# Optimization experiments

Hardware: AMD Instinct MI355X
Metric: run time of the kernel (lower is better)

Reference implementation:

```python
import jax, jax.numpy as jnp
import numpy as np

T, B_SZ = 1024, 1024
NX, NU, ND, NM, NDT, NH = 128, 64, 32, 32, 32, 128


def setup_inputs() -> dict:
    key = jax.random.key(0)
    ks = jax.random.split(key, 10)
    return {
        "x": jax.random.normal(ks[0], (B_SZ, NX), jnp.float32),
        "M_flow": jax.random.normal(ks[1], (T, B_SZ, NM), jnp.float32),
        "DT": jax.random.normal(ks[2], (T, B_SZ, NDT), jnp.float32),
        "D": jax.random.normal(ks[3], (T, B_SZ, ND), jnp.float32),
        # ConstrainedLinear(nx, nx): weight and scalar init with torch.rand -> uniform[0,1)
        "A_weight": jax.random.uniform(ks[4], (NX, NX), jnp.float32),
        "A_scalar": jax.random.uniform(ks[5], (NX, NX), jnp.float32),
        # nn.Linear(in, out, bias=False) weights are [out, in]
        "B_w": jax.random.normal(ks[6], (NX, NU), jnp.float32) * (1.0 / np.sqrt(NU)),
        "E_w": jax.random.normal(ks[7], (NX, ND), jnp.float32) * (1.0 / np.sqrt(ND)),
        "hf1_w": jax.random.normal(ks[8], (NH, NM + NDT), jnp.float32) * (1.0 / np.sqrt(NM + NDT)),
        "hf2_w": jax.random.normal(ks[9], (NU, NH), jnp.float32) * (1.0 / np.sqrt(NH)),
    }


def reference(x, M_flow, DT, D, A_weight, A_scalar, B_w, E_w, hf1_w, hf2_w):
    # Constrained weight: ((1 - 0.1*sigmoid(scalar)) * softmax(weight, dim=1)).T
    # It is constant across time, so compute once (torch redundantly recomputes it per step).
    s_clamped = 1.0 - 0.1 * jax.nn.sigmoid(A_scalar)
    W_eff = (s_clamped * jax.nn.softmax(A_weight, axis=1)).T  # [nx, nx]

    # Per-step control input u_t depends only on exogenous M_flow/DT -> vectorize over time.
    md = jnp.concatenate([M_flow, DT], axis=2)                # [T, B, n_m+n_dT]
    h = jax.nn.relu(jnp.einsum('tbi,hi->tbh', md, hf1_w))     # [T, B, n_hidden]
    u = jax.nn.relu(jnp.einsum('tbh,uh->tbu', h, hf2_w))      # [T, B, nu]

    # Precompute additive drive B(u_t) + E(d_t); only x@W_eff is sequential.
    drive = jnp.einsum('tbu,xu->tbx', u, B_w) + jnp.einsum('tbd,xd->tbx', D, E_w)

    def step(x_prev, drive_t):
        x_new = x_prev @ W_eff + drive_t
        return x_new, x_new

    _, X = jax.lax.scan(step, x, drive)  # X: [T, B, nx]
    Y = X[:, :, -1]                      # [T, B]
    return X, Y
```

## Files before the change

### kernel.cpp

```cpp
#include <hip/hip_runtime.h>

typedef _Float16 h4 __attribute__((ext_vector_type(4)));
typedef _Float16 h8 __attribute__((ext_vector_type(8)));
typedef float f4 __attribute__((ext_vector_type(4)));

#define MFMA16(a, b, c) __builtin_amdgcn_mfma_f32_16x16x32_f16((a), (b), (c), 0, 0, 0)

static constexpr int TT  = 1024;
static constexpr int BS  = 1024;
static constexpr int LCH = 32;
static constexpr int NCH = 32;
static constexpr size_t XTOT = (size_t)TT * BS * 128;

static constexpr size_t WS_WT16 = 0;
static constexpr size_t WS_HF1  = 32768;
static constexpr size_t WS_HF2  = 49152;
static constexpr size_t WS_BW   = 65536;
static constexpr size_t WS_EW   = 81920;
static constexpr size_t WS_W32  = 90112;
static constexpr size_t WS_F    = 131072;
static constexpr size_t WS_INIT = WS_F + (size_t)NCH * BS * 128 * 4;
static constexpr size_t WS_DRV  = WS_INIT + (size_t)NCH * BS * 128 * 4;

template <typename T>
__device__ inline T ntload(const T* p) { return __builtin_nontemporal_load(p); }

__global__ void prep_kernel(const float* __restrict__ Aw, const float* __restrict__ As,
                            const float* __restrict__ hf1, const float* __restrict__ hf2,
                            const float* __restrict__ Bw, const float* __restrict__ Ew,
                            char* __restrict__ ws)
{
    const int tid = threadIdx.x;
    const int bid = blockIdx.x;
    if (bid < 128) {
        __shared__ float red[128];
        const int n = bid;
        const float a = Aw[n * 128 + tid];
        red[tid] = a;
        __syncthreads();
        for (int s = 64; s > 0; s >>= 1) {
            if (tid < s) red[tid] = fmaxf(red[tid], red[tid + s]);
            __syncthreads();
        }
        const float mx = red[0];
        __syncthreads();
        const float e = expf(a - mx);
        red[tid] = e;
        __syncthreads();
        for (int s = 64; s > 0; s >>= 1) {
            if (tid < s) red[tid] += red[tid + s];
            __syncthreads();
        }
        const float sm  = e / red[0];
        const float asv = As[n * 128 + tid];
        const float sc  = 1.0f - 0.1f * (1.0f / (1.0f + expf(-asv)));
        ((_Float16*)(ws + WS_WT16))[n * 128 + tid] = (_Float16)(sc * sm);
    } else {
        const int b2 = bid - 128;
        for (int i = b2 * 128 + tid; i < 8192; i += 32 * 128) {
            ((_Float16*)(ws + WS_HF1))[i] = (_Float16)hf1[i];
            ((_Float16*)(ws + WS_HF2))[i] = (_Float16)hf2[i];
            ((_Float16*)(ws + WS_BW))[i]  = (_Float16)Bw[i];
            if (i < 4096) ((_Float16*)(ws + WS_EW))[i] = (_Float16)Ew[i];
        }
    }
}

__global__ void w32_kernel(char* __restrict__ ws)
{
    const int tid  = threadIdx.x;
    const int lane = tid & 63;
    const int w    = tid >> 6;
    const int cl   = lane & 15;
    const int gq   = lane >> 4;

    __shared__ __align__(16) _Float16 Ta[128 * 128];
    __shared__ __align__(16) _Float16 Tb[128 * 128];

    const _Float16* Wt16 = (const _Float16*)(ws + WS_WT16);
    for (int i = tid; i < 2048; i += 256)
        *(h8*)&Ta[i * 8] = *(const h8*)&Wt16[i * 8];
    __syncthreads();

    for (int s = 0; s < 5; ++s) {
        const _Float16* src = (s & 1) ? Tb : Ta;
        _Float16* dst       = (s & 1) ? Ta : Tb;
        f4 acc[8][2];
#pragma unroll
        for (int mt = 0; mt < 8; ++mt)
#pragma unroll
            for (int nt = 0; nt < 2; ++nt) acc[mt][nt] = f4{};
#pragma unroll
        for (int kk = 0; kk < 4; ++kk) {
            h8 b0, b1;
#pragma unroll
            for (int j = 0; j < 8; ++j) {
                const int kr = kk * 32 + gq * 8 + j;
                b0[j] = src[kr * 128 + w * 32 + cl];
                b1[j] = src[kr * 128 + w * 32 + 16 + cl];
            }
#pragma unroll
            for (int mt = 0; mt < 8; ++mt) {
                h8 a = *(const h8*)&src[(mt * 16 + cl) * 128 + kk * 32 + gq * 8];
                acc[mt][0] = MFMA16(a, b0, acc[mt][0]);
                acc[mt][1] = MFMA16(a, b1, acc[mt][1]);
            }
        }
        __syncthreads();
#pragma unroll
        for (int mt = 0; mt < 8; ++mt)
#pragma unroll
            for (int nt = 0; nt < 2; ++nt)
#pragma unroll
                for (int r = 0; r < 4; ++r)
                    dst[(mt * 16 + gq * 4 + r) * 128 + w * 32 + nt * 16 + cl] =
                        (_Float16)acc[mt][nt][r];
        __syncthreads();
    }
    _Float16* W32 = (_Float16*)(ws + WS_W32);
    for (int i = tid; i < 2048; i += 256)
        *(h8*)&W32[i * 8] = *(const h8*)&Tb[i * 8];
}

__global__ __launch_bounds__(256, 4)
void drive_kernel(const float* __restrict__ Mfl, const float* __restrict__ DTi,
                  const float* __restrict__ Din, char* __restrict__ ws)
{
    const int tid  = threadIdx.x;
    const int lane = tid & 63;
    const int w    = tid >> 6;
    const int cl   = lane & 15;
    const int gq   = lane >> 4;
    const int bt   = blockIdx.x & 63;
    const int tq   = blockIdx.x >> 6;
    const int b0   = bt * 16;

    const _Float16* Hf1  = (const _Float16*)(ws + WS_HF1);
    const _Float16* Hf2  = (const _Float16*)(ws + WS_HF2);
    const _Float16* Bw16 = (const _Float16*)(ws + WS_BW);
    const _Float16* Ew16 = (const _Float16*)(ws + WS_EW);
    _Float16* Drv        = (_Float16*)(ws + WS_DRV);

    __shared__ __align__(16) _Float16 mds[4][16 * 64];
    __shared__ __align__(16) _Float16 dts[4][16 * 32];
    __shared__ __align__(16) _Float16 hs[4][16 * 128];
    __shared__ __align__(16) _Float16 us[4][16 * 64];

    const int qrow = (tid & 127) >> 3;
    const int qc4  = (tid & 7) * 4;
    f4 pm[4], pd[4];
#pragma unroll
    for (int s = 0; s < 4; ++s) {
        const size_t t  = (size_t)tq * 4 + s;
        const size_t rb = (t * BS + b0 + qrow) * 32 + qc4;
        pm[s] = (tid < 128) ? ntload((const f4*)&Mfl[rb]) : ntload((const f4*)&DTi[rb]);
        if (tid < 128) pd[s] = ntload((const f4*)&Din[rb]);
    }
#pragma unroll
    for (int s = 0; s < 4; ++s) {
        const int col = (tid < 128) ? qc4 : (32 + qc4);
        h4 hv;
#pragma unroll
        for (int j = 0; j < 4; ++j) hv[j] = (_Float16)pm[s][j];
        *(h4*)&mds[s][qrow * 64 + (((col >> 3) ^ (qrow & 7)) * 8) + (col & 7)] = hv;
        if (tid < 128) {
            h4 h2;
#pragma unroll
            for (int j = 0; j < 4; ++j) h2[j] = (_Float16)pd[s][j];
            *(h4*)&dts[s][qrow * 32 + (((qc4 >> 3) ^ (qrow & 3)) * 8) + (qc4 & 7)] = h2;
        }
    }

    h8 hf1f[2][2], bwf[2][2], ewf[2], hf2f[4];
#pragma unroll
    for (int nt = 0; nt < 2; ++nt) {
        const int ng = w * 32 + nt * 16 + cl;
#pragma unroll
        for (int kk = 0; kk < 2; ++kk) {
            hf1f[nt][kk] = *(const h8*)&Hf1[ng * 64 + kk * 32 + gq * 8];
            bwf[nt][kk]  = *(const h8*)&Bw16[ng * 64 + kk * 32 + gq * 8];
        }
        ewf[nt] = *(const h8*)&Ew16[ng * 32 + gq * 8];
    }
    {
        const int ng = w * 16 + cl;
#pragma unroll
        for (int kk = 0; kk < 4; ++kk)
            hf2f[kk] = *(const h8*)&Hf2[ng * 128 + kk * 32 + gq * 8];
    }
    __syncthreads();

#pragma unroll
    for (int s = 0; s < 4; ++s) {
        f4 ha[2] = {};
#pragma unroll
        for (int kk = 0; kk < 2; ++kk) {
            h8 a = *(const h8*)&mds[s][cl * 64 + (((kk * 4 + gq) ^ (cl & 7)) * 8)];
            ha[0] = MFMA16(hf1f[0][kk], a, ha[0]);
            ha[1] = MFMA16(hf1f[1][kk], a, ha[1]);
        }
#pragma unroll
        for (int nt = 0; nt < 2; ++nt) {
            const int nb8 = w * 4 + nt * 2 + (gq >> 1);
            h4 hv;
#pragma unroll
            for (int r = 0; r < 4; ++r) hv[r] = (_Float16)fmaxf(ha[nt][r], 0.f);
            *(h4*)&hs[s][cl * 128 + ((nb8 ^ cl) & 15) * 8 + (gq & 1) * 4] = hv;
        }
    }
    __syncthreads();

#pragma unroll
    for (int s = 0; s < 4; ++s) {
        f4 ua = {};
#pragma unroll
        for (int kt = 0; kt < 4; ++kt) {
            h8 a = *(const h8*)&hs[s][cl * 128 + (((kt * 4 + gq) ^ cl) & 15) * 8];
            ua = MFMA16(hf2f[kt], a, ua);
        }
        const int nb8 = w * 2 + (gq >> 1);
        h4 hv;
#pragma unroll
        for (int r = 0; r < 4; ++r) hv[r] = (_Float16)fmaxf(ua[r], 0.f);
        *(h4*)&us[s][cl * 64 + ((nb8 ^ (cl & 7)) & 7) * 8 + (gq & 1) * 4] = hv;
    }
    __syncthreads();

#pragma unroll
    for (int s = 0; s < 4; ++s) {
        f4 acc[2] = {};
#pragma unroll
        for (int kk = 0; kk < 2; ++kk) {
            h8 a = *(const h8*)&us[s][cl * 64 + (((kk * 4 + gq) ^ (cl & 7)) & 7) * 8];
            acc[0] = MFMA16(bwf[0][kk], a, acc[0]);
            acc[1] = MFMA16(bwf[1][kk], a, acc[1]);
        }
        {
            h8 a = *(const h8*)&dts[s][cl * 32 + ((gq ^ (cl & 3)) * 8)];
            acc[0] = MFMA16(ewf[0], a, acc[0]);
            acc[1] = MFMA16(ewf[1], a, acc[1]);
        }
        h8 o;
#pragma unroll
        for (int r = 0; r < 4; ++r) { o[r] = (_Float16)acc[0][r]; o[4 + r] = (_Float16)acc[1][r]; }
        const size_t t = (size_t)tq * 4 + s;
        *(h8*)&Drv[((t * 64 + bt) * 256 + tid) * 8] = o;
    }
}

template <bool FINAL>
__global__ __launch_bounds__(256, 2)
void scan_kernel(char* __restrict__ ws,
                 float* __restrict__ Xout, float* __restrict__ Yout)
{
    const int wslot = threadIdx.x >> 6;
    const int wid   = blockIdx.x * 4 + wslot;
    const int lane  = threadIdx.x & 63;
    const int cl = lane & 15, gq = lane >> 4;
    const int c  = wid >> 6;
    const int bt = wid & 63;
    const int b0 = bt * 16;

    const _Float16* Wt16 = (const _Float16*)(ws + WS_WT16);
    const _Float16* Drv  = (const _Float16*)(ws + WS_DRV);
    float* Fbuf       = (float*)(ws + WS_F);
    const float* Init = (const float*)(ws + WS_INIT);

    __shared__ __align__(16) _Float16 tb[4][16 * 128];
    _Float16* tbuf = tb[wslot];

    h8 wf[8][4];
#pragma unroll
    for (int nt = 0; nt < 8; ++nt)
#pragma unroll
        for (int kt = 0; kt < 4; ++kt)
            wf[nt][kt] = *(const h8*)&Wt16[(nt * 16 + cl) * 128 + kt * 32 + gq * 8];

    h8 xf[4];
    if constexpr (FINAL) {
        f4 iv[8];
#pragma unroll
        for (int nt = 0; nt < 8; ++nt)
            iv[nt] = *(const f4*)&Init[((size_t)c * BS + b0 + cl) * 128 + nt * 16 + gq * 4];
#pragma unroll
        for (int nt = 0; nt < 8; ++nt) {
            h4 hv;
#pragma unroll
            for (int r = 0; r < 4; ++r) hv[r] = (_Float16)iv[nt][r];
            *(h4*)&tbuf[cl * 128 + (((nt * 2 + (gq >> 1)) ^ cl) & 15) * 8 + (gq & 1) * 4] = hv;
        }
#pragma unroll
        for (int kt = 0; kt < 4; ++kt)
            xf[kt] = *(const h8*)&tbuf[cl * 128 + (((kt * 4 + gq) ^ cl) & 15) * 8];
    } else {
#pragma unroll
        for (int kt = 0; kt < 4; ++kt) xf[kt] = h8{};
    }

    constexpr size_t STEP = 16384;
    const h8* dp = (const h8*)Drv + (((size_t)(c * LCH) * 64 + bt) * 4) * 64 + lane;
    h8 dra0, dra1, dra2, dra3, drb0, drb1, drb2, drb3;
    dra0 = dp[0];          dra1 = dp[64];          dra2 = dp[128];          dra3 = dp[192];
    drb0 = dp[STEP];       drb1 = dp[STEP + 64];   drb2 = dp[STEP + 128];   drb3 = dp[STEP + 192];

#define SCAN_STEP(K, D0, D1, D2, D3)                                                     \
    {                                                                                    \
        f4 acc[8];                                                                       \
        _Pragma("unroll") for (int r = 0; r < 4; ++r) {                                  \
            acc[0][r] = (float)D0[r]; acc[1][r] = (float)D0[4 + r];                      \
            acc[2][r] = (float)D1[r]; acc[3][r] = (float)D1[4 + r];                      \
            acc[4][r] = (float)D2[r]; acc[5][r] = (float)D2[4 + r];                      \
            acc[6][r] = (float)D3[r]; acc[7][r] = (float)D3[4 + r];                      \
        }                                                                                \
        if ((K) + 2 < LCH) {                                                             \
            D0 = dp[(size_t)((K) + 2) * STEP + 0];                                       \
            D1 = dp[(size_t)((K) + 2) * STEP + 64];                                      \
            D2 = dp[(size_t)((K) + 2) * STEP + 128];                                     \
            D3 = dp[(size_t)((K) + 2) * STEP + 192];                                     \
        }                                                                                \
        _Pragma("unroll") for (int kt = 0; kt < 4; ++kt)                                 \
            _Pragma("unroll") for (int nt = 0; nt < 8; ++nt)                             \
                acc[nt] = MFMA16(wf[nt][kt], xf[kt], acc[nt]);                           \
        if constexpr (FINAL) {                                                           \
            const size_t t = (size_t)c * LCH + (K);                                      \
            float* xp = &Xout[(t * BS + b0 + cl) * 128 + gq * 4];                        \
            _Pragma("unroll") for (int nt = 0; nt < 8; ++nt)                             \
                __builtin_nontemporal_store(acc[nt], (f4*)&xp[nt * 16]);                 \
            if (gq == 3)                                                                 \
                __builtin_nontemporal_store(acc[7][3], &Yout[t * BS + b0 + cl]);         \
        } else if ((K) == LCH - 1) {                                                     \
            _Pragma("unroll") for (int nt = 0; nt < 8; ++nt)                             \
                *(f4*)&Fbuf[((size_t)c * BS + b0 + cl) * 128 + nt * 16 + gq * 4] =       \
                    acc[nt];                                                             \
        }                                                                                \
        if ((K) < LCH - 1) {                                                             \
            _Pragma("unroll") for (int nt = 0; nt < 8; ++nt) {                           \
                h4 hv;                                                                   \
                _Pragma("unroll") for (int r = 0; r < 4; ++r)                            \
                    hv[r] = (_Float16)acc[nt][r];                                        \
                *(h4*)&tbuf[cl * 128 + (((nt * 2 + (gq >> 1)) ^ cl) & 15) * 8 +          \
                            (gq & 1) * 4] = hv;                                          \
            }                                                                            \
            _Pragma("unroll") for (int kt = 0; kt < 4; ++kt)                             \
                xf[kt] = *(const h8*)&tbuf[cl * 128 + (((kt * 4 + gq) ^ cl) & 15) * 8];  \
        }                                                                                \
    }

    for (int k = 0; k < LCH; k += 2) {
        SCAN_STEP(k, dra0, dra1, dra2, dra3);
        SCAN_STEP(k + 1, drb0, drb1, drb2, drb3);
    }
#undef SCAN_STEP
}

__global__ __launch_bounds__(64, 1)
void carry_kernel(const float* __restrict__ x0, char* __restrict__ ws, int n_steps)
{
    const int lane = threadIdx.x;
    const int cl = lane & 15, gq = lane >> 4;
    const int b0 = blockIdx.x * 16;

    const _Float16* W32 = (const _Float16*)(ws + WS_W32);
    const float* Fbuf   = (const float*)(ws + WS_F);
    float* Init         = (float*)(ws + WS_INIT);

    __shared__ __align__(16) _Float16 tbuf[16 * 128];

    h8 wf[8][4];
#pragma unroll
    for (int nt = 0; nt < 8; ++nt)
#pragma unroll
        for (int kt = 0; kt < 4; ++kt)
            wf[nt][kt] = *(const h8*)&W32[(nt * 16 + cl) * 128 + kt * 32 + gq * 8];

    h8 xf[4];
    {
        f4 iv[8];
#pragma unroll
        for (int nt = 0; nt < 8; ++nt)
            iv[nt] = *(const f4*)&x0[(size_t)(b0 + cl) * 128 + nt * 16 + gq * 4];
#pragma unroll
        for (int nt = 0; nt < 8; ++nt)
            *(f4*)&Init[(size_t)(b0 + cl) * 128 + nt * 16 + gq * 4] = iv[nt];
#pragma unroll
        for (int nt = 0; nt < 8; ++nt) {
            h4 hv;
#pragma unroll
            for (int r = 0; r < 4; ++r) hv[r] = (_Float16)iv[nt][r];
            *(h4*)&tbuf[cl * 128 + (((nt * 2 + (gq >> 1)) ^ cl) & 15) * 8 + (gq & 1) * 4] = hv;
        }
#pragma unroll
        for (int kt = 0; kt < 4; ++kt)
            xf[kt] = *(const h8*)&tbuf[cl * 128 + (((kt * 4 + gq) ^ cl) & 15) * 8];
    }

    for (int cc = 1; cc <= n_steps; ++cc) {
        f4 acc[8];
#pragma unroll
        for (int nt = 0; nt < 8; ++nt)
            acc[nt] = *(const f4*)&Fbuf[((size_t)(cc - 1) * BS + b0 + cl) * 128 + nt * 16 + gq * 4];
#pragma unroll
        for (int kt = 0; kt < 4; ++kt)
#pragma unroll
            for (int nt = 0; nt < 8; ++nt)
                acc[nt] = MFMA16(wf[nt][kt], xf[kt], acc[nt]);
#pragma unroll
        for (int nt = 0; nt < 8; ++nt)
            *(f4*)&Init[((size_t)cc * BS + b0 + cl) * 128 + nt * 16 + gq * 4] = acc[nt];
        if (cc < n_steps) {
#pragma unroll
            for (int nt = 0; nt < 8; ++nt) {
                h4 hv;
#pragma unroll
                for (int r = 0; r < 4; ++r) hv[r] = (_Float16)acc[nt][r];
                *(h4*)&tbuf[cl * 128 + (((nt * 2 + (gq >> 1)) ^ cl) & 15) * 8 + (gq & 1) * 4] = hv;
            }
#pragma unroll
            for (int kt = 0; kt < 4; ++kt)
                xf[kt] = *(const h8*)&tbuf[cl * 128 + (((kt * 4 + gq) ^ cl) & 15) * 8];
        }
    }
}

extern "C" void kernel_launch(void* const* d_in, const int* in_sizes, int n_in,
                              void* d_out, int out_size, void* d_ws, size_t ws_size,
                              hipStream_t stream)
{
    const float* x_in = (const float*)d_in[0];
    const float* Mfl  = (const float*)d_in[1];
    const float* DTi  = (const float*)d_in[2];
    const float* Din  = (const float*)d_in[3];
    const float* Aw   = (const float*)d_in[4];
    const float* As   = (const float*)d_in[5];
    const float* Bw   = (const float*)d_in[6];
    const float* Ew   = (const float*)d_in[7];
    const float* hf1  = (const float*)d_in[8];
    const float* hf2  = (const float*)d_in[9];
    char* ws    = (char*)d_ws;
    float* Xout = (float*)d_out;
    float* Yout = Xout + XTOT;

    prep_kernel<<<dim3(160), dim3(128), 0, stream>>>(Aw, As, hf1, hf2, Bw, Ew, ws);
    w32_kernel<<<dim3(1), dim3(256), 0, stream>>>(ws);

    drive_kernel<<<dim3(256 * 64), dim3(256), 0, stream>>>(Mfl, DTi, Din, ws);
    scan_kernel<false><<<dim3(496), dim3(256), 0, stream>>>(ws, nullptr, nullptr);
    carry_kernel<<<dim3(64), dim3(64), 0, stream>>>(x_in, ws, 31);
    scan_kernel<true><<<dim3(512), dim3(256), 0, stream>>>(ws, Xout, Yout);
}
```

Baseline: 456.0 us.

## Fuse drive computation into chunked scan kernels and drop drive buffer

Removes the separate drive kernel and its fp16 drive buffer in workspace. Each scan block now recomputes the MLP drive for its chunk on the fly, with its 4 waves splitting the output columns and syncing through shared memory each step. The chunk scan runs twice (partial and final), so the drive MLP is computed twice and the per-step block barrier adds latency. In exchange, a large global write and read of drive data is avoided. The W^32 power kernel is also reworked to keep both transposed copies in padded shared memory so B-operand loads vectorize.

```diff
diff --git a/kernel.cpp b/kernel.cpp
--- a/kernel.cpp
+++ b/kernel.cpp
@@ -20,7 +20,6 @@
 static constexpr size_t WS_W32  = 90112;
 static constexpr size_t WS_F    = 131072;
 static constexpr size_t WS_INIT = WS_F + (size_t)NCH * BS * 128 * 4;
-static constexpr size_t WS_DRV  = WS_INIT + (size_t)NCH * BS * 128 * 4;
 
 template <typename T>
 __device__ inline T ntload(const T* p) { return __builtin_nontemporal_load(p); }
@@ -73,58 +72,76 @@
     const int w    = tid >> 6;
     const int cl   = lane & 15;
     const int gq   = lane >> 4;
-
-    __shared__ __align__(16) _Float16 Ta[128 * 128];
-    __shared__ __align__(16) _Float16 Tb[128 * 128];
+    constexpr int LDP = 136;
+
+    __shared__ __align__(16) _Float16 G[2][128 * LDP];
+    __shared__ __align__(16) _Float16 H[2][128 * LDP];
 
     const _Float16* Wt16 = (const _Float16*)(ws + WS_WT16);
     for (int i = tid; i < 2048; i += 256)
-        *(h8*)&Ta[i * 8] = *(const h8*)&Wt16[i * 8];
+        *(h8*)&G[0][(i >> 4) * LDP + (i & 15) * 8] = *(const h8*)&Wt16[i * 8];
     __syncthreads();
-
+    for (int i = tid; i < 16384; i += 256) {
+        const int r = i >> 7, cc = i & 127;
+        H[0][cc * LDP + r] = G[0][r * LDP + cc];
+    }
+    __syncthreads();
+
+    int cur = 0;
     for (int s = 0; s < 5; ++s) {
-        const _Float16* src = (s & 1) ? Tb : Ta;
-        _Float16* dst       = (s & 1) ? Ta : Tb;
-        f4 acc[8][2];
+        const _Float16* Gs = G[cur];
+        const _Float16* Hs = H[cur];
+        _Float16* Gd = G[cur ^ 1];
+        _Float16* Hd = H[cur ^ 1];
+        f4 aG[8][2], aH[8][2];
 #pragma unroll
         for (int mt = 0; mt < 8; ++mt)
 #pragma unroll
-            for (int nt = 0; nt < 2; ++nt) acc[mt][nt] = f4{};
+            for (int nt = 0; nt < 2; ++nt) { aG[mt][nt] = f4{}; aH[mt][nt] = f4{}; }
 #pragma unroll
         for (int kk = 0; kk < 4; ++kk) {
-            h8 b0, b1;
-#pragma unroll
-            for (int j = 0; j < 8; ++j) {
-                const int kr = kk * 32 + gq * 8 + j;
-                b0[j] = src[kr * 128 + w * 32 + cl];
-                b1[j] = src[kr * 128 + w * 32 + 16 + cl];
-            }
+            h8 bG0 = *(const h8*)&Hs[((w * 2 + 0) * 16 + cl) * LDP + kk * 32 + gq * 8];
+            h8 bG1 = *(const h8*)&Hs[((w * 2 + 1) * 16 + cl) * LDP + kk * 32 + gq * 8];
+            h8 bH0 = *(const h8*)&Gs[((w * 2 + 0) * 16 + cl) * LDP + kk * 32 + gq * 8];
+            h8 bH1 = *(const h8*)&Gs[((w * 2 + 1) * 16 + cl) * LDP + kk * 32 + gq * 8];
 #pragma unroll
             for (int mt = 0; mt < 8; ++mt) {
-                h8 a = *(const h8*)&src[(mt * 16 + cl) * 128 + kk * 32 + gq * 8];
-                acc[mt][0] = MFMA16(a, b0, acc[mt][0]);
-                acc[mt][1] = MFMA16(a, b1, acc[mt][1]);
-            }
-        }
-        __syncthreads();
+                h8 ag = *(const h8*)&Gs[(mt * 16 + cl) * LDP + kk * 32 + gq * 8];
+                h8 ah = *(const h8*)&Hs[(mt * 16 + cl) * LDP + kk * 32 + gq * 8];
+                aG[mt][0] = MFMA16(ag, bG0, aG[mt][0]);
+                aG[mt][1] = MFMA16(ag, bG1, aG[mt][1]);
+                aH[mt][0] = MFMA16(ah, bH0, aH[mt][0]);
+                aH[mt][1] = MFMA16(ah, bH1, aH[mt][1]);
+            }
+        }
 #pragma unroll
         for (int mt = 0; mt < 8; ++mt)
 #pragma unroll
-            for (int nt = 0; nt < 2; ++nt)
-#pragma unroll
-                for (int r = 0; r < 4; ++r)
-                    dst[(mt * 16 + gq * 4 + r) * 128 + w * 32 + nt * 16 + cl] =
-                        (_Float16)acc[mt][nt][r];
-        __syncthreads();
+            for (int nt = 0; nt < 2; ++nt) {
+                h4 hg, hh;
+#pragma unroll
+                for (int r = 0; r < 4; ++r) {
+                    hg[r] = (_Float16)aG[mt][nt][r];
+                    hh[r] = (_Float16)aH[mt][nt][r];
+                }
+                const int col  = (w * 2 + nt) * 16 + cl;
+                const int rowb = mt * 16 + gq * 4;
+                *(h4*)&Hd[col * LDP + rowb] = hg;
+                *(h4*)&Gd[col * LDP + rowb] = hh;
+            }
+        __syncthreads();
+        cur ^= 1;
     }
     _Float16* W32 = (_Float16*)(ws + WS_W32);
     for (int i = tid; i < 2048; i += 256)
-        *(h8*)&W32[i * 8] = *(const h8*)&Tb[i * 8];
+        *(h8*)&W32[i * 8] = *(const h8*)&G[cur][(i >> 4) * LDP + (i & 15) * 8];
 }
 
-__global__ __launch_bounds__(256, 4)
-void drive_kernel(const float* __restrict__ Mfl, const float* __restrict__ DTi,
-                  const float* __restrict__ Din, char* __restrict__ ws)
+template <bool FINAL>
+__global__ __launch_bounds__(256, 2)
+void fused_scan(const float* __restrict__ Mfl, const float* __restrict__ DTi,
+                const float* __restrict__ Din, char* __restrict__ ws,
+                float* __restrict__ Xout, float* __restrict__ Yout)
 {
     const int tid  = threadIdx.x;
     const int lane = tid & 63;
@@ -132,229 +149,206 @@
     const int cl   = lane & 15;
     const int gq   = lane >> 4;
     const int bt   = blockIdx.x & 63;
-    const int tq   = blockIdx.x >> 6;
+    const int c    = blockIdx.x >> 6;
     const int b0   = bt * 16;
 
     const _Float16* Hf1  = (const _Float16*)(ws + WS_HF1);
     const _Float16* Hf2  = (const _Float16*)(ws + WS_HF2);
     const _Float16* Bw16 = (const _Float16*)(ws + WS_BW);
     const _Float16* Ew16 = (const _Float16*)(ws + WS_EW);
-    _Float16* Drv        = (_Float16*)(ws + WS_DRV);
+    const _Float16* Wt16 = (const _Float16*)(ws + WS_WT16);
+    float* Fbuf          = (float*)(ws + WS_F);
+    const float* Init    = (const float*)(ws + WS_INIT);
 
     __shared__ __align__(16) _Float16 mds[4][16 * 64];
     __shared__ __align__(16) _Float16 dts[4][16 * 32];
     __shared__ __align__(16) _Float16 hs[4][16 * 128];
     __shared__ __align__(16) _Float16 us[4][16 * 64];
+    __shared__ __align__(16) _Float16 xsh[2][16 * 128];
+
+    h8 hf1f[2][2], bwf[2][2], ewf[2], hf2f[4];
+#pragma unroll
+    for (int nt = 0; nt < 2; ++nt) {
+        const int ng = w * 32 + nt * 16 + cl;
+#pragma unroll
+        for (int kk = 0; kk < 2; ++kk) {
+            hf1f[nt][kk] = *(const h8*)&Hf1[ng * 64 + kk * 32 + gq * 8];
+            bwf[nt][kk]  = *(const h8*)&Bw16[ng * 64 + kk * 32 + gq * 8];
+        }
+        ewf[nt] = *(const h8*)&Ew16[ng * 32 + gq * 8];
+    }
+    {
+        const int ng = w * 16 + cl;
+#pragma unroll
+        for (int kk = 0; kk < 4; ++kk)
+            hf2f[kk] = *(const h8*)&Hf2[ng * 128 + kk * 32 + gq * 8];
+    }
+    h8 wfp[2][4];
+#pragma unroll
+    for (int nt = 0; nt < 2; ++nt)
+#pragma unroll
+        for (int kt = 0; kt < 4; ++kt)
+            wfp[nt][kt] =
+                *(const h8*)&Wt16[(w * 32 + nt * 16 + cl) * 128 + kt * 32 + gq * 8];
+
+    if constexpr (FINAL) {
+        const int row = tid >> 4, c8 = tid & 15;
+        const float* src = &Init[((size_t)c * BS + b0 + row) * 128 + c8 * 8];
+        f4 v0 = *(const f4*)src, v1 = *(const f4*)(src + 4);
+        h8 hv;
+#pragma unroll
+        for (int j = 0; j < 4; ++j) { hv[j] = (_Float16)v0[j]; hv[4 + j] = (_Float16)v1[j]; }
+        *(h8*)&xsh[0][row * 128 + ((c8 ^ row) & 15) * 8] = hv;
+    } else {
+        h8 z = {};
+        *(h8*)&xsh[0][tid * 8] = z;
+    }
 
     const int qrow = (tid & 127) >> 3;
     const int qc4  = (tid & 7) * 4;
     f4 pm[4], pd[4];
-#pragma unroll
-    for (int s = 0; s < 4; ++s) {
-        const size_t t  = (size_t)tq * 4 + s;
-        const size_t rb = (t * BS + b0 + qrow) * 32 + qc4;
-        pm[s] = (tid < 128) ? ntload((const f4*)&Mfl[rb]) : ntload((const f4*)&DTi[rb]);
-        if (tid < 128) pd[s] = ntload((const f4*)&Din[rb]);
-    }
-#pragma unroll
-    for (int s = 0; s < 4; ++s) {
-        const int col = (tid < 128) ? qc4 : (32 + qc4);
-        h4 hv;
-#pragma unroll
-        for (int j = 0; j < 4; ++j) hv[j] = (_Float16)pm[s][j];
-        *(h4*)&mds[s][qrow * 64 + (((col >> 3) ^ (qrow & 7)) * 8) + (col & 7)] = hv;
-        if (tid < 128) {
-            h4 h2;
-#pragma unroll
-            for (int j = 0; j < 4; ++j) h2[j] = (_Float16)pd[s][j];
-            *(h4*)&dts[s][qrow * 32 + (((qc4 >> 3) ^ (qrow & 3)) * 8) + (qc4 & 7)] = h2;
-        }
-    }
-
-    h8 hf1f[2][2], bwf[2][2], ewf[2], hf2f[4];
-#pragma unroll
-    for (int nt = 0; nt < 2; ++nt) {
-        const int ng = w * 32 + nt * 16 + cl;
-#pragma unroll
-        for (int kk = 0; kk < 2; ++kk) {
-            hf1f[nt][kk] = *(const h8*)&Hf1[ng * 64 + kk * 32 + gq * 8];
-            bwf[nt][kk]  = *(const h8*)&Bw16[ng * 64 + kk * 32 + gq * 8];
-        }
-        ewf[nt] = *(const h8*)&Ew16[ng * 32 + gq * 8];
-    }
-    {
-        const int ng = w * 16 + cl;
-#pragma unroll
-        for (int kk = 0; kk < 4; ++kk)
-            hf2f[kk] = *(const h8*)&Hf2[ng * 128 + kk * 32 + gq * 8];
-    }
-    __syncthreads();
-
-#pragma unroll
-    for (int s = 0; s < 4; ++s) {
-        f4 ha[2] = {};
-#pragma unroll
-        for (int kk = 0; kk < 2; ++kk) {
-            h8 a = *(const h8*)&mds[s][cl * 64 + (((kk * 4 + gq) ^ (cl & 7)) * 8)];
-            ha[0] = MFMA16(hf1f[0][kk], a, ha[0]);
-            ha[1] = MFMA16(hf1f[1][kk], a, ha[1]);
-        }
-#pragma unroll
-        for (int nt = 0; nt < 2; ++nt) {
-            const int nb8 = w * 4 + nt * 2 + (gq >> 1);
+    auto GLOAD = [&](int g) {
+#pragma unroll
+        for (int s = 0; s < 4; ++s) {
+            const size_t t  = (size_t)c * LCH + g * 4 + s;
+            const size_t rb = (t * BS + b0 + qrow) * 32 + qc4;
+            pm[s] = (tid < 128) ? ntload((const f4*)&Mfl[rb]) : ntload((const f4*)&DTi[rb]);
+            if (tid < 128) pd[s] = ntload((const f4*)&Din[rb]);
+        }
+    };
+    GLOAD(0);
+
+    _Float16* xcur = xsh[0];
+    _Float16* xnxt = xsh[1];
+
+    for (int g = 0; g < 8; ++g) {
+#pragma unroll
+        for (int s = 0; s < 4; ++s) {
+            const int col = (tid < 128) ? qc4 : (32 + qc4);
             h4 hv;
 #pragma unroll
-            for (int r = 0; r < 4; ++r) hv[r] = (_Float16)fmaxf(ha[nt][r], 0.f);
-            *(h4*)&hs[s][cl * 128 + ((nb8 ^ cl) & 15) * 8 + (gq & 1) * 4] = hv;
-        }
-    }
-    __syncthreads();
-
-#pragma unroll
-    for (int s = 0; s < 4; ++s) {
-        f4 ua = {};
-#pragma unroll
-        for (int kt = 0; kt < 4; ++kt) {
-            h8 a = *(const h8*)&hs[s][cl * 128 + (((kt * 4 + gq) ^ cl) & 15) * 8];
-            ua = MFMA16(hf2f[kt], a, ua);
-        }
-        const int nb8 = w * 2 + (gq >> 1);
-        h4 hv;
-#pragma unroll
-        for (int r = 0; r < 4; ++r) hv[r] = (_Float16)fmaxf(ua[r], 0.f);
-        *(h4*)&us[s][cl * 64 + ((nb8 ^ (cl & 7)) & 7) * 8 + (gq & 1) * 4] = hv;
-    }
-    __syncthreads();
-
-#pragma unroll
-    for (int s = 0; s < 4; ++s) {
-        f4 acc[2] = {};
-#pragma unroll
-        for (int kk = 0; kk < 2; ++kk) {
-            h8 a = *(const h8*)&us[s][cl * 64 + (((kk * 4 + gq) ^ (cl & 7)) & 7) * 8];
-            acc[0] = MFMA16(bwf[0][kk], a, acc[0]);
-            acc[1] = MFMA16(bwf[1][kk], a, acc[1]);
-        }
-        {
-            h8 a = *(const h8*)&dts[s][cl * 32 + ((gq ^ (cl & 3)) * 8)];
-            acc[0] = MFMA16(ewf[0], a, acc[0]);
-            acc[1] = MFMA16(ewf[1], a, acc[1]);
-        }
-        h8 o;
-#pragma unroll
-        for (int r = 0; r < 4; ++r) { o[r] = (_Float16)acc[0][r]; o[4 + r] = (_Float16)acc[1][r]; }
-        const size_t t = (size_t)tq * 4 + s;
-        *(h8*)&Drv[((t * 64 + bt) * 256 + tid) * 8] = o;
+            for (int j = 0; j < 4; ++j) hv[j] = (_Float16)pm[s][j];
+            *(h4*)&mds[s][qrow * 64 + (((col >> 3) ^ (qrow & 7)) * 8) + (col & 7)] = hv;
+            if (tid < 128) {
+                h4 h2;
+#pragma unroll
+                for (int j = 0; j < 4; ++j) h2[j] = (_Float16)pd[s][j];
+                *(h4*)&dts[s][qrow * 32 + (((qc4 >> 3) ^ (qrow & 3)) * 8) + (qc4 & 7)] = h2;
+            }
+        }
+        if (g < 7) GLOAD(g + 1);
+        __syncthreads();
+
+#pragma unroll
+        for (int s = 0; s < 4; ++s) {
+            f4 ha0 = {}, ha1 = {};
+#pragma unroll
+            for (int kk = 0; kk < 2; ++kk) {
+                h8 a = *(const h8*)&mds[s][cl * 64 + (((kk * 4 + gq) ^ (cl & 7)) * 8)];
+                ha0 = MFMA16(hf1f[0][kk], a, ha0);
+                ha1 = MFMA16(hf1f[1][kk], a, ha1);
+            }
+#pragma unroll
+            for (int nt = 0; nt < 2; ++nt) {
+                const int nb8 = w * 4 + nt * 2 + (gq >> 1);
+                h4 hv;
+#pragma unroll
+                for (int r = 0; r < 4; ++r)
+                    hv[r] = (_Float16)fmaxf(nt ? ha1[r] : ha0[r], 0.f);
+                *(h4*)&hs[s][cl * 128 + ((nb8 ^ cl) & 15) * 8 + (gq & 1) * 4] = hv;
+            }
+        }
+        __syncthreads();
+
+#pragma unroll
+        for (int s = 0; s < 4; ++s) {
+            f4 ua = {};
+#pragma unroll
+            for (int kt = 0; kt < 4; ++kt) {
+                h8 a = *(const h8*)&hs[s][cl * 128 + (((kt * 4 + gq) ^ cl) & 15) * 8];
+                ua = MFMA16(hf2f[kt], a, ua);
+            }
+            const int ub8 = w * 2 + (gq >> 1);
+            h4 uv;
+#pragma unroll
+            for (int r = 0; r < 4; ++r) uv[r] = (_Float16)fmaxf(ua[r], 0.f);
+            *(h4*)&us[s][cl * 64 + ((ub8 ^ (cl & 7)) & 7) * 8 + (gq & 1) * 4] = uv;
+        }
+        __syncthreads();
+
+        h4 dv[4][2];
+#pragma unroll
+        for (int s = 0; s < 4; ++s) {
+            f4 a20 = {}, a21 = {};
+#pragma unroll
+            for (int kk = 0; kk < 2; ++kk) {
+                h8 a = *(const h8*)&us[s][cl * 64 + (((kk * 4 + gq) ^ (cl & 7)) & 7) * 8];
+                a20 = MFMA16(bwf[0][kk], a, a20);
+                a21 = MFMA16(bwf[1][kk], a, a21);
+            }
+            {
+                h8 ad = *(const h8*)&dts[s][cl * 32 + ((gq ^ (cl & 3)) * 8)];
+                a20 = MFMA16(ewf[0], ad, a20);
+                a21 = MFMA16(ewf[1], ad, a21);
+            }
+#pragma unroll
+            for (int r = 0; r < 4; ++r) {
+                dv[s][0][r] = (_Float16)a20[r];
+                dv[s][1][r] = (_Float16)a21[r];
+            }
+        }
+
+#pragma unroll
+        for (int s = 0; s < 4; ++s) {
+            h8 xf[4];
+#pragma unroll
+            for (int kt = 0; kt < 4; ++kt)
+                xf[kt] = *(const h8*)&xcur[cl * 128 + (((kt * 4 + gq) ^ cl) & 15) * 8];
+            f4 acc0, acc1;
+#pragma unroll
+            for (int r = 0; r < 4; ++r) {
+                acc0[r] = (float)dv[s][0][r];
+                acc1[r] = (float)dv[s][1][r];
+            }
+#pragma unroll
+            for (int kt = 0; kt < 4; ++kt) {
+                acc0 = MFMA16(wfp[0][kt], xf[kt], acc0);
+                acc1 = MFMA16(wfp[1][kt], xf[kt], acc1);
+            }
+
+            if constexpr (FINAL) {
+                const size_t t = (size_t)c * LCH + g * 4 + s;
+                float* xp = &Xout[(t * BS + b0 + cl) * 128 + w * 32 + gq * 4];
+                __builtin_nontemporal_store(acc0, (f4*)xp);
+                __builtin_nontemporal_store(acc1, (f4*)(xp + 16));
+                if (w == 3 && gq == 3)
+                    __builtin_nontemporal_store(acc1[3], &Yout[t * BS + b0 + cl]);
+            }
+            const bool last = (g == 7) && (s == 3);
+            if (!FINAL && last) {
+                float* fp = &Fbuf[((size_t)c * BS + b0 + cl) * 128 + w * 32 + gq * 4];
+                *(f4*)fp = acc0;
+                *(f4*)(fp + 16) = acc1;
+            }
+            if (!last) {
+#pragma unroll
+                for (int nt = 0; nt < 2; ++nt) {
+                    h4 hv;
+#pragma unroll
+                    for (int r = 0; r < 4; ++r) hv[r] = (_Float16)(nt ? acc1[r] : acc0[r]);
+                    const int nb8 = w * 4 + nt * 2 + (gq >> 1);
+                    *(h4*)&xnxt[cl * 128 + ((nb8 ^ cl) & 15) * 8 + (gq & 1) * 4] = hv;
+                }
+                __syncthreads();
+                _Float16* tmp = xcur; xcur = xnxt; xnxt = tmp;
+            }
+        }
     }
 }
 
-template <bool FINAL>
-__global__ __launch_bounds__(256, 2)
-void scan_kernel(char* __restrict__ ws,
-                 float* __restrict__ Xout, float* __restrict__ Yout)
-{
-    const int wslot = threadIdx.x >> 6;
-    const int wid   = blockIdx.x * 4 + wslot;
-    const int lane  = threadIdx.x & 63;
-    const int cl = lane & 15, gq = lane >> 4;
-    const int c  = wid >> 6;
-    const int bt = wid & 63;
-    const int b0 = bt * 16;
-
-    const _Float16* Wt16 = (const _Float16*)(ws + WS_WT16);
-    const _Float16* Drv  = (const _Float16*)(ws + WS_DRV);
-    float* Fbuf       = (float*)(ws + WS_F);
-    const float* Init = (const float*)(ws + WS_INIT);
-
-    __shared__ __align__(16) _Float16 tb[4][16 * 128];
-    _Float16* tbuf = tb[wslot];
-
-    h8 wf[8][4];
-#pragma unroll
-    for (int nt = 0; nt < 8; ++nt)
-#pragma unroll
-        for (int kt = 0; kt < 4; ++kt)
-            wf[nt][kt] = *(const h8*)&Wt16[(nt * 16 + cl) * 128 + kt * 32 + gq * 8];
-
-    h8 xf[4];
-    if constexpr (FINAL) {
-        f4 iv[8];
-#pragma unroll
-        for (int nt = 0; nt < 8; ++nt)
-            iv[nt] = *(const f4*)&Init[((size_t)c * BS + b0 + cl) * 128 + nt * 16 + gq * 4];
-#pragma unroll
-        for (int nt = 0; nt < 8; ++nt) {
-            h4 hv;
-#pragma unroll
-            for (int r = 0; r < 4; ++r) hv[r] = (_Float16)iv[nt][r];
-            *(h4*)&tbuf[cl * 128 + (((nt * 2 + (gq >> 1)) ^ cl) & 15) * 8 + (gq & 1) * 4] = hv;
-        }
-#pragma unroll
-        for (int kt = 0; kt < 4; ++kt)
-            xf[kt] = *(const h8*)&tbuf[cl * 128 + (((kt * 4 + gq) ^ cl) & 15) * 8];
-    } else {
-#pragma unroll
-        for (int kt = 0; kt < 4; ++kt) xf[kt] = h8{};
-    }
-
-    constexpr size_t STEP = 16384;
-    const h8* dp = (const h8*)Drv + (((size_t)(c * LCH) * 64 + bt) * 4) * 64 + lane;
-    h8 dra0, dra1, dra2, dra3, drb0, drb1, drb2, drb3;
-    dra0 = dp[0];          dra1 = dp[64];          dra2 = dp[128];          dra3 = dp[192];
-    drb0 = dp[STEP];       drb1 = dp[STEP + 64];   drb2 = dp[STEP + 128];   drb3 = dp[STEP + 192];
-
-#define SCAN_STEP(K, D0, D1, D2, D3)                                                     \
-    {                                                                                    \
-        f4 acc[8];                                                                       \
-        _Pragma("unroll") for (int r = 0; r < 4; ++r) {                                  \
-            acc[0][r] = (float)D0[r]; acc[1][r] = (float)D0[4 + r];                      \
-            acc[2][r] = (float)D1[r]; acc[3][r] = (float)D1[4 + r];                      \
-            acc[4][r] = (float)D2[r]; acc[5][r] = (float)D2[4 + r];                      \
-            acc[6][r] = (float)D3[r]; acc[7][r] = (float)D3[4 + r];                      \
-        }                                                                                \
-        if ((K) + 2 < LCH) {                                                             \
-            D0 = dp[(size_t)((K) + 2) * STEP + 0];                                       \
-            D1 = dp[(size_t)((K) + 2) * STEP + 64];                                      \
-            D2 = dp[(size_t)((K) + 2) * STEP + 128];                                     \
-            D3 = dp[(size_t)((K) + 2) * STEP + 192];                                     \
-        }                                                                                \
-        _Pragma("unroll") for (int kt = 0; kt < 4; ++kt)                                 \
-            _Pragma("unroll") for (int nt = 0; nt < 8; ++nt)                             \
-                acc[nt] = MFMA16(wf[nt][kt], xf[kt], acc[nt]);                           \
-        if constexpr (FINAL) {                                                           \
-            const size_t t = (size_t)c * LCH + (K);                                      \
-            float* xp = &Xout[(t * BS + b0 + cl) * 128 + gq * 4];                        \
-            _Pragma("unroll") for (int nt = 0; nt < 8; ++nt)                             \
-                __builtin_nontemporal_store(acc[nt], (f4*)&xp[nt * 16]);                 \
-            if (gq == 3)                                                                 \
-                __builtin_nontemporal_store(acc[7][3], &Yout[t * BS + b0 + cl]);         \
-        } else if ((K) == LCH - 1) {                                                     \
-            _Pragma("unroll") for (int nt = 0; nt < 8; ++nt)                             \
-                *(f4*)&Fbuf[((size_t)c * BS + b0 + cl) * 128 + nt * 16 + gq * 4] =       \
-                    acc[nt];                                                             \
-        }                                                                                \
-        if ((K) < LCH - 1) {                                                             \
-            _Pragma("unroll") for (int nt = 0; nt < 8; ++nt) {                           \
-                h4 hv;                                                                   \
-                _Pragma("unroll") for (int r = 0; r < 4; ++r)                            \
-                    hv[r] = (_Float16)acc[nt][r];                                        \
-                *(h4*)&tbuf[cl * 128 + (((nt * 2 + (gq >> 1)) ^ cl) & 15) * 8 +          \
-                            (gq & 1) * 4] = hv;                                          \
-            }                                                                            \
-            _Pragma("unroll") for (int kt = 0; kt < 4; ++kt)                             \
-                xf[kt] = *(const h8*)&tbuf[cl * 128 + (((kt * 4 + gq) ^ cl) & 15) * 8];  \
-        }                                                                                \
-    }
-
-    for (int k = 0; k < LCH; k += 2) {
-        SCAN_STEP(k, dra0, dra1, dra2, dra3);
-        SCAN_STEP(k + 1, drb0, drb1, drb2, drb3);
-    }
-#undef SCAN_STEP
-}
-
 __global__ __launch_bounds__(64, 1)
-void carry_kernel(const float* __restrict__ x0, char* __restrict__ ws, int n_steps)
+void carry_kernel(const float* __restrict__ x0, char* __restrict__ ws,
+                  int cc_lo, int n_steps, int copy0)
 {
     const int lane = threadIdx.x;
     const int cl = lane & 15, gq = lane >> 4;
@@ -379,9 +373,11 @@
 #pragma unroll
         for (int nt = 0; nt < 8; ++nt)
             iv[nt] = *(const f4*)&x0[(size_t)(b0 + cl) * 128 + nt * 16 + gq * 4];
-#pragma unroll
-        for (int nt = 0; nt < 8; ++nt)
-            *(f4*)&Init[(size_t)(b0 + cl) * 128 + nt * 16 + gq * 4] = iv[nt];
+        if (copy0) {
+#pragma unroll
+            for (int nt = 0; nt < 8; ++nt)
+                *(f4*)&Init[((size_t)cc_lo * BS + b0 + cl) * 128 + nt * 16 + gq * 4] = iv[nt];
+        }
 #pragma unroll
         for (int nt = 0; nt < 8; ++nt) {
             h4 hv;
@@ -394,7 +390,8 @@
             xf[kt] = *(const h8*)&tbuf[cl * 128 + (((kt * 4 + gq) ^ cl) & 15) * 8];
     }
 
-    for (int cc = 1; cc <= n_steps; ++cc) {
+    for (int i = 1; i <= n_steps; ++i) {
+        const int cc = cc_lo + i;
         f4 acc[8];
 #pragma unroll
         for (int nt = 0; nt < 8; ++nt)
@@ -407,7 +404,7 @@
 #pragma unroll
         for (int nt = 0; nt < 8; ++nt)
             *(f4*)&Init[((size_t)cc * BS + b0 + cl) * 128 + nt * 16 + gq * 4] = acc[nt];
-        if (cc < n_steps) {
+        if (i < n_steps) {
 #pragma unroll
             for (int nt = 0; nt < 8; ++nt) {
                 h4 hv;
@@ -443,8 +440,9 @@
     prep_kernel<<<dim3(160), dim3(128), 0, stream>>>(Aw, As, hf1, hf2, Bw, Ew, ws);
     w32_kernel<<<dim3(1), dim3(256), 0, stream>>>(ws);
 
-    drive_kernel<<<dim3(256 * 64), dim3(256), 0, stream>>>(Mfl, DTi, Din, ws);
-    scan_kernel<false><<<dim3(496), dim3(256), 0, stream>>>(ws, nullptr, nullptr);
-    carry_kernel<<<dim3(64), dim3(64), 0, stream>>>(x_in, ws, 31);
-    scan_kernel<true><<<dim3(512), dim3(256), 0, stream>>>(ws, Xout, Yout);
+    fused_scan<false><<<dim3(31 * 64), dim3(256), 0, stream>>>(Mfl, DTi, Din, ws,
+                                                               nullptr, nullptr);
+    carry_kernel<<<dim3(64), dim3(64), 0, stream>>>(x_in, ws, 0, 31, 1);
+    fused_scan<true><<<dim3(32 * 64), dim3(256), 0, stream>>>(Mfl, DTi, Din, ws,
+                                                              Xout, Yout);
 }
```

Result: faster. 422.8 us (-7.3%).
